# Kernel optimization log

Measured on AMD Instinct MI355X. Metric: run time of the kernel, lower is better.

Reference implementation:

```python
import jax, jax.numpy as jnp
import numpy as np
import math

H = 16
D_MODEL = 1024
D_K = D_MODEL // H


def setup_inputs() -> dict:
    key = jax.random.key(0)
    ks = jax.random.split(key, 12)
    B, S = 4, 2048
    inp = {
        "query": jax.random.normal(ks[0], (B, S, D_MODEL), jnp.float32),
        "key": jax.random.normal(ks[1], (B, S, D_MODEL), jnp.float32),
        "value": jax.random.normal(ks[2], (B, S, D_MODEL), jnp.float32),
        # causal mask, broadcastable over heads: [B, 1, S, S]
        "mask": jnp.broadcast_to(jnp.tril(jnp.ones((S, S), bool)), (B, 1, S, S)),
    }
    sc = 1.0 / math.sqrt(D_MODEL)
    inp["Wq"] = jax.random.normal(ks[3], (D_MODEL, D_MODEL), jnp.float32) * sc
    inp["bq"] = jnp.zeros((D_MODEL,), jnp.float32)
    inp["Wk"] = jax.random.normal(ks[4], (D_MODEL, D_MODEL), jnp.float32) * sc
    inp["bk"] = jnp.zeros((D_MODEL,), jnp.float32)
    inp["Wv"] = jax.random.normal(ks[5], (D_MODEL, D_MODEL), jnp.float32) * sc
    inp["bv"] = jnp.zeros((D_MODEL,), jnp.float32)
    inp["Wo"] = jax.random.normal(ks[6], (D_MODEL, D_MODEL), jnp.float32) * sc
    inp["bo"] = jnp.zeros((D_MODEL,), jnp.float32)
    return inp


def reference(query, key, value, mask, Wq, bq, Wk, bk, Wv, bv, Wo, bo):
    B, S, D = query.shape
    # torch nn.Linear: y = x @ W.T + b; then view(B,-1,h,d_k).transpose(1,2)
    def proj(x, W, b):
        return (x @ W.T + b).reshape(B, -1, H, D_K).transpose(0, 2, 1, 3)  # [B,h,S,d_k]

    q = proj(query, Wq, bq)
    k = proj(key, Wk, bk)
    v = proj(value, Wv, bv)

    scores = jnp.einsum("bhqd,bhkd->bhqk", q, k) / math.sqrt(D_K)
    scores = jnp.where(mask, scores, jnp.finfo(scores.dtype).min)
    p_attn = jax.nn.softmax(scores, axis=-1)  # dropout: eval mode (identity)
    x = jnp.einsum("bhqk,bhkd->bhqd", p_attn, v)
    x = x.transpose(0, 2, 1, 3).reshape(B, -1, H * D_K)
    return x @ Wo.T + bo
```

## Files before the change

kernel.cpp:

```cpp
#include <hip/hip_runtime.h>
#include <hip/hip_bf16.h>

typedef unsigned short u16;
typedef __attribute__((ext_vector_type(8))) short short8;
typedef __attribute__((ext_vector_type(4))) short short4v;
typedef __attribute__((ext_vector_type(4))) float f32x4;
typedef __attribute__((ext_vector_type(4))) float float4_t;

#define DIM 1024
#define NH  16
#define DKK 64
#define SEQ 2048
#define NB  4
#define SM_SCALE 0.1803368801111244f

__device__ __forceinline__ u16 f2bf(float f) {
    __bf16 h = (__bf16)f;
    return __builtin_bit_cast(u16, h);
}

__device__ __forceinline__ f32x4 mfma_bf16(short8 a, short8 b, f32x4 c) {
    return __builtin_amdgcn_mfma_f32_16x16x32_bf16(a, b, c, 0, 0, 0);
}

__device__ __forceinline__ short8 ld8_lds(const u16* p) {
    short4v lo = *(const short4v*)p;
    short4v hi = *(const short4v*)(p + 4);
    return __builtin_shufflevector(lo, hi, 0, 1, 2, 3, 4, 5, 6, 7);
}

__device__ __forceinline__ void st8_lds(u16* p, short8 v) {
    *(short4v*)p       = __builtin_shufflevector(v, v, 0, 1, 2, 3);
    *(short4v*)(p + 4) = __builtin_shufflevector(v, v, 4, 5, 6, 7);
}

__device__ __forceinline__ short8 pack8(float4_t a, float4_t b) {
    short8 v;
    v[0] = (short)f2bf(a[0]); v[1] = (short)f2bf(a[1]);
    v[2] = (short)f2bf(a[2]); v[3] = (short)f2bf(a[3]);
    v[4] = (short)f2bf(b[0]); v[5] = (short)f2bf(b[1]);
    v[6] = (short)f2bf(b[2]); v[7] = (short)f2bf(b[3]);
    return v;
}

template<int MODE>
__global__ __launch_bounds__(256)
void gemm128(const float* __restrict__ Afp, const u16* __restrict__ Abf,
             const float* __restrict__ W, const float* __restrict__ bias,
             u16* __restrict__ Cbf, float* __restrict__ Cf)
{
    __shared__ u16 As[128][40];
    __shared__ u16 Bs[128][40];
    const int tid  = threadIdx.x;
    const int lane = tid & 63;
    const int wid  = tid >> 6;
    const int wr   = wid >> 1, wc = wid & 1;
    const int m0   = blockIdx.y * 128;
    const int n0   = blockIdx.x * 128;
    const int lm   = lane & 15, lg = lane >> 4;

    f32x4 acc[4][4];
#pragma unroll
    for (int i = 0; i < 4; ++i)
#pragma unroll
        for (int j = 0; j < 4; ++j) acc[i][j] = (f32x4){0.f, 0.f, 0.f, 0.f};

    for (int k0 = 0; k0 < DIM; k0 += 32) {
#pragma unroll
        for (int it = 0; it < 2; ++it) {
            const int c   = tid + it * 256;
            const int row = c >> 2, seg = c & 3;
            short8 va;
            if (MODE == 1) {
                va = *(const short8*)(Abf + (size_t)(row + m0) * DIM + k0 + seg * 8);
            } else {
                const float* s = Afp + (size_t)(row + m0) * DIM + k0 + seg * 8;
                va = pack8(*(const float4_t*)s, *(const float4_t*)(s + 4));
            }
            st8_lds(&As[row][seg * 8], va);
            const float* sw = W + (size_t)(row + n0) * DIM + k0 + seg * 8;
            st8_lds(&Bs[row][seg * 8], pack8(*(const float4_t*)sw, *(const float4_t*)(sw + 4)));
        }
        __syncthreads();

        short8 af[4], bfr[4];
#pragma unroll
        for (int t = 0; t < 4; ++t) {
            af[t]  = ld8_lds(&As[wr * 64 + t * 16 + lm][lg * 8]);
            bfr[t] = ld8_lds(&Bs[wc * 64 + t * 16 + lm][lg * 8]);
        }
#pragma unroll
        for (int mt = 0; mt < 4; ++mt)
#pragma unroll
            for (int nt = 0; nt < 4; ++nt)
                acc[mt][nt] = mfma_bf16(af[mt], bfr[nt], acc[mt][nt]);
        __syncthreads();
    }

#pragma unroll
    for (int mt = 0; mt < 4; ++mt)
#pragma unroll
        for (int nt = 0; nt < 4; ++nt)
#pragma unroll
            for (int r = 0; r < 4; ++r) {
                const int m = m0 + wr * 64 + mt * 16 + lg * 4 + r;
                const int n = n0 + wc * 64 + nt * 16 + lm;
                if (MODE == 0) {
                    const float val = acc[mt][nt][r] + bias[n];
                    const int b = m >> 11, s = m & 2047;
                    const int h = n >> 6,  dk = n & 63;
                    Cbf[(((size_t)b * NH + h) * SEQ + s) * DKK + dk] = f2bf(val);
                } else if (MODE == 1) {
                    Cf[(size_t)m * DIM + n] = acc[mt][nt][r] + bias[n];
                } else {
                    const float val = acc[mt][nt][r] + bias[m];
                    const int h = m >> 6, dk = m & 63;
                    const int b = n >> 11, s = n & 2047;
                    Cbf[(((size_t)b * NH + h) * DKK + dk) * SEQ + s] = f2bf(val);
                }
            }
}

__global__ __launch_bounds__(256, 2)
void attn3(const u16* __restrict__ Q, const u16* __restrict__ K,
           const u16* __restrict__ Vt, u16* __restrict__ O)
{
    __shared__ __align__(16) u16 Ks[64][72];
    __shared__ __align__(16) u16 Vs[64][72];
    __shared__ __align__(16) u16 Ps[4][32][72];

    const int tid  = threadIdx.x;
    const int lane = tid & 63;
    const int w    = tid >> 6;
    const int lm   = lane & 15, lg = lane >> 4;
    const int pb   = blockIdx.x;
    const int bh   = blockIdx.y;
    const int Abase = pb * 64;
    const int Bbase = SEQ - 64 - Abase;
    const int qA = Abase + 16 * w;
    const int qB = Bbase + 16 * w;
    const u16* Qp = Q  + (size_t)bh * SEQ * DKK;
    const u16* Kp = K  + (size_t)bh * SEQ * DKK;
    const u16* Vp = Vt + (size_t)bh * DKK * SEQ;

    short8 qa[2][2];
#pragma unroll
    for (int kh = 0; kh < 2; ++kh) {
        qa[0][kh] = *(const short8*)(Qp + (size_t)(qA + lm) * DKK + kh * 32 + lg * 8);
        qa[1][kh] = *(const short8*)(Qp + (size_t)(qB + lm) * DKK + kh * 32 + lg * 8);
    }

    float m_q[2] = {-INFINITY, -INFINITY};
    float l_q[2] = {0.f, 0.f};
    f32x4 o[2][4];
#pragma unroll
    for (int qt = 0; qt < 2; ++qt)
#pragma unroll
        for (int dt = 0; dt < 4; ++dt) o[qt][dt] = (f32x4){0.f, 0.f, 0.f, 0.f};

    const f32x4 zero = (f32x4){0.f, 0.f, 0.f, 0.f};
    const int srow = tid >> 3;
    const int soct = (tid & 7) * 8;
    const int kv_end = Bbase + 64;

    short8 rk0 = *(const short8*)(Kp + (size_t)srow * DKK + soct);
    short8 rk1 = *(const short8*)(Kp + (size_t)(srow + 32) * DKK + soct);
    short8 rv0 = *(const short8*)(Vp + (size_t)srow * SEQ + soct);
    short8 rv1 = *(const short8*)(Vp + (size_t)(srow + 32) * SEQ + soct);

    for (int kv0 = 0; kv0 < kv_end; kv0 += 64) {
        __syncthreads();
        *(short8*)&Ks[srow][soct]      = rk0;
        *(short8*)&Ks[srow + 32][soct] = rk1;
        *(short8*)&Vs[srow][soct]      = rv0;
        *(short8*)&Vs[srow + 32][soct] = rv1;
        const int nkv = kv0 + 64;
        if (nkv < kv_end) {
            rk0 = *(const short8*)(Kp + (size_t)(nkv + srow) * DKK + soct);
            rk1 = *(const short8*)(Kp + (size_t)(nkv + srow + 32) * DKK + soct);
            rv0 = *(const short8*)(Vp + (size_t)srow * SEQ + nkv + soct);
            rv1 = *(const short8*)(Vp + (size_t)(srow + 32) * SEQ + nkv + soct);
        }
        __syncthreads();

        const bool actA = kv0 < qA + 16;
        const bool msk[2] = { kv0 + 63 > qA, kv0 + 63 > qB };
        const bool act[2] = { actA, true };
        const int  qb[2]  = { qA, qB };

        f32x4 s[2][4];
#pragma unroll
        for (int kvt = 0; kvt < 4; ++kvt) {
            const short8 kb0 = *(const short8*)&Ks[kvt * 16 + lm][lg * 8];
            const short8 kb1 = *(const short8*)&Ks[kvt * 16 + lm][32 + lg * 8];
            s[1][kvt] = mfma_bf16(kb1, qa[1][1], mfma_bf16(kb0, qa[1][0], zero));
            if (actA)
                s[0][kvt] = mfma_bf16(kb1, qa[0][1], mfma_bf16(kb0, qa[0][0], zero));
        }

        float mx[2] = {-INFINITY, -INFINITY};
#pragma unroll
        for (int qt = 0; qt < 2; ++qt) {
            if (!act[qt]) continue;
#pragma unroll
            for (int kvt = 0; kvt < 4; ++kvt)
#pragma unroll
                for (int r = 0; r < 4; ++r) s[qt][kvt][r] *= SM_SCALE;
            if (msk[qt]) {
                const int q = qb[qt] + lm;
#pragma unroll
                for (int kvt = 0; kvt < 4; ++kvt)
#pragma unroll
                    for (int r = 0; r < 4; ++r) {
                        const int kv = kv0 + kvt * 16 + lg * 4 + r;
                        if (kv > q) s[qt][kvt][r] = -INFINITY;
                    }
            }
            float vmax = -INFINITY;
#pragma unroll
            for (int kvt = 0; kvt < 4; ++kvt)
#pragma unroll
                for (int r = 0; r < 4; ++r) vmax = fmaxf(vmax, s[qt][kvt][r]);
            vmax = fmaxf(vmax, __shfl_xor(vmax, 16));
            vmax = fmaxf(vmax, __shfl_xor(vmax, 32));
            mx[qt] = vmax;
        }

        const bool small = (!actA || mx[0] <= m_q[0] + 8.f) && (mx[1] <= m_q[1] + 8.f);
        if (__all(small)) {
#pragma unroll
            for (int qt = 0; qt < 2; ++qt) {
                if (!act[qt]) continue;
                float ls = 0.f;
#pragma unroll
                for (int kvt = 0; kvt < 4; ++kvt) {
                    short4v pk;
#pragma unroll
                    for (int r = 0; r < 4; ++r) {
                        const float p = __builtin_exp2f(s[qt][kvt][r] - m_q[qt]);
                        ls += p;
                        pk[r] = (short)f2bf(p);
                    }
                    *(short4v*)&Ps[w][qt * 16 + lm][kvt * 16 + lg * 4] = pk;
                }
                l_q[qt] += ls;
            }
        } else {
#pragma unroll
            for (int qt = 0; qt < 2; ++qt) {
                if (!act[qt]) continue;
                const float mnew = fmaxf(m_q[qt], mx[qt]);
                const float alpha = __builtin_exp2f(m_q[qt] - mnew);
                m_q[qt] = mnew;
                float ls = 0.f;
#pragma unroll
                for (int kvt = 0; kvt < 4; ++kvt) {
                    short4v pk;
#pragma unroll
                    for (int r = 0; r < 4; ++r) {
                        const float p = __builtin_exp2f(s[qt][kvt][r] - mnew);
                        ls += p;
                        pk[r] = (short)f2bf(p);
                    }
                    *(short4v*)&Ps[w][qt * 16 + lm][kvt * 16 + lg * 4] = pk;
                }
                l_q[qt] = l_q[qt] * alpha + ls;
#pragma unroll
                for (int r = 0; r < 4; ++r) {
                    const float ar = __shfl(alpha, lg * 4 + r);
#pragma unroll
                    for (int dt = 0; dt < 4; ++dt) o[qt][dt][r] *= ar;
                }
            }
        }
        asm volatile("s_waitcnt lgkmcnt(0)" ::: "memory");

        short8 pa[2][2], vbt[4][2];
#pragma unroll
        for (int qt = 0; qt < 2; ++qt)
            if (act[qt]) {
                pa[qt][0] = *(const short8*)&Ps[w][qt * 16 + lm][lg * 8];
                pa[qt][1] = *(const short8*)&Ps[w][qt * 16 + lm][32 + lg * 8];
            }
#pragma unroll
        for (int dt = 0; dt < 4; ++dt) {
            vbt[dt][0] = *(const short8*)&Vs[dt * 16 + lm][lg * 8];
            vbt[dt][1] = *(const short8*)&Vs[dt * 16 + lm][32 + lg * 8];
        }
#pragma unroll
        for (int dt = 0; dt < 4; ++dt)
#pragma unroll
            for (int qt = 0; qt < 2; ++qt) {
                if (!act[qt]) continue;
                o[qt][dt] = mfma_bf16(pa[qt][1], vbt[dt][1],
                                      mfma_bf16(pa[qt][0], vbt[dt][0], o[qt][dt]));
            }
    }

    const int b = bh >> 4, h = bh & 15;
#pragma unroll
    for (int qt = 0; qt < 2; ++qt) {
        float lf = l_q[qt];
        lf += __shfl_xor(lf, 16);
        lf += __shfl_xor(lf, 32);
        const int qbase = qt ? qB : qA;
#pragma unroll
        for (int r = 0; r < 4; ++r) {
            const float li = 1.f / __shfl(lf, lg * 4 + r);
            const int srw = qbase + lg * 4 + r;
#pragma unroll
            for (int dt = 0; dt < 4; ++dt)
                O[(((size_t)b * SEQ + srw) * NH + h) * DKK + dt * 16 + lm] =
                    f2bf(o[qt][dt][r] * li);
        }
    }
}

extern "C" void kernel_launch(void* const* d_in, const int* in_sizes, int n_in,
                              void* d_out, int out_size, void* d_ws, size_t ws_size,
                              hipStream_t stream)
{
    const float* query = (const float*)d_in[0];
    const float* key   = (const float*)d_in[1];
    const float* value = (const float*)d_in[2];
    const float* Wq = (const float*)d_in[4];
    const float* bq = (const float*)d_in[5];
    const float* Wk = (const float*)d_in[6];
    const float* bk = (const float*)d_in[7];
    const float* Wv = (const float*)d_in[8];
    const float* bv = (const float*)d_in[9];
    const float* Wo = (const float*)d_in[10];
    const float* bo = (const float*)d_in[11];
    float* out = (float*)d_out;

    const size_t HD = (size_t)NB * NH * SEQ * DKK;
    u16* qws  = (u16*)d_ws;
    u16* kws  = qws + HD;
    u16* vtws = kws + HD;
    u16* ows  = vtws + HD;

    dim3 gg(DIM / 128, (NB * SEQ) / 128);
    dim3 gv((NB * SEQ) / 128, DIM / 128);
    gemm128<0><<<gg, 256, 0, stream>>>(query, nullptr, Wq, bq, qws, nullptr);
    gemm128<0><<<gg, 256, 0, stream>>>(key,   nullptr, Wk, bk, kws, nullptr);
    gemm128<2><<<gv, 256, 0, stream>>>(Wv, nullptr, value, bv, vtws, nullptr);
    attn3<<<dim3(SEQ / 128, NB * NH), 256, 0, stream>>>(qws, kws, vtws, ows);
    gemm128<1><<<gg, 256, 0, stream>>>(nullptr, ows, Wo, bo, nullptr, out);
}
```

Measured before the change: 264.6 us.

## Use direct global-to-LDS loads with swizzled fp32 staging in projection GEMMs

```diff
diff --git a/kernel.cpp b/kernel.cpp
--- a/kernel.cpp
+++ b/kernel.cpp
@@ -2,6 +2,7 @@
 #include <hip/hip_bf16.h>
 
 typedef unsigned short u16;
+typedef unsigned int u32;
 typedef __attribute__((ext_vector_type(8))) short short8;
 typedef __attribute__((ext_vector_type(4))) short short4v;
 typedef __attribute__((ext_vector_type(4))) float f32x4;
@@ -21,17 +22,6 @@
 
 __device__ __forceinline__ f32x4 mfma_bf16(short8 a, short8 b, f32x4 c) {
     return __builtin_amdgcn_mfma_f32_16x16x32_bf16(a, b, c, 0, 0, 0);
-}
-
-__device__ __forceinline__ short8 ld8_lds(const u16* p) {
-    short4v lo = *(const short4v*)p;
-    short4v hi = *(const short4v*)(p + 4);
-    return __builtin_shufflevector(lo, hi, 0, 1, 2, 3, 4, 5, 6, 7);
-}
-
-__device__ __forceinline__ void st8_lds(u16* p, short8 v) {
-    *(short4v*)p       = __builtin_shufflevector(v, v, 0, 1, 2, 3);
-    *(short4v*)(p + 4) = __builtin_shufflevector(v, v, 4, 5, 6, 7);
 }
 
 __device__ __forceinline__ short8 pack8(float4_t a, float4_t b) {
@@ -43,22 +33,34 @@
     return v;
 }
 
+typedef const __attribute__((address_space(1))) u32* gas1_t;
+typedef __attribute__((address_space(3))) u32* las3_t;
+__device__ __forceinline__ void g2l16(const void* g, void* l) {
+    __builtin_amdgcn_global_load_lds((gas1_t)g, (las3_t)l, 16, 0, 0);
+}
+
 template<int MODE>
 __global__ __launch_bounds__(256)
 void gemm128(const float* __restrict__ Afp, const u16* __restrict__ Abf,
              const float* __restrict__ W, const float* __restrict__ bias,
              u16* __restrict__ Cbf, float* __restrict__ Cf)
 {
-    __shared__ u16 As[128][40];
-    __shared__ u16 Bs[128][40];
+    __shared__ __align__(16) char AsRaw[MODE == 1 ? 8192 : 16384];
+    __shared__ __align__(16) float Bs[128 * 32];
+
     const int tid  = threadIdx.x;
     const int lane = tid & 63;
-    const int wid  = tid >> 6;
-    const int wr   = wid >> 1, wc = wid & 1;
+    const int w    = tid >> 6;
+    const int wr   = w >> 1, wc = w & 1;
     const int m0   = blockIdx.y * 128;
     const int n0   = blockIdx.x * 128;
     const int lm   = lane & 15, lg = lane >> 4;
 
+    const int fr = tid >> 3;
+    const int fc = (tid & 7) ^ ((tid >> 3) & 7);
+    const int hr = tid >> 2;
+    const int hc = (tid & 3) ^ ((tid >> 3) & 3);
+
     f32x4 acc[4][4];
 #pragma unroll
     for (int i = 0; i < 4; ++i)
@@ -66,35 +68,54 @@
         for (int j = 0; j < 4; ++j) acc[i][j] = (f32x4){0.f, 0.f, 0.f, 0.f};
 
     for (int k0 = 0; k0 < DIM; k0 += 32) {
-#pragma unroll
-        for (int it = 0; it < 2; ++it) {
-            const int c   = tid + it * 256;
-            const int row = c >> 2, seg = c & 3;
-            short8 va;
+        __syncthreads();
+        if (MODE == 1) {
+#pragma unroll
+            for (int c = 0; c < 2; ++c)
+                g2l16(Abf + (size_t)(m0 + c * 64 + hr) * DIM + k0 + hc * 8,
+                      AsRaw + c * 4096 + w * 1024);
+        } else {
+#pragma unroll
+            for (int c = 0; c < 4; ++c)
+                g2l16(Afp + (size_t)(m0 + c * 32 + fr) * DIM + k0 + fc * 4,
+                      AsRaw + c * 4096 + w * 1024);
+        }
+#pragma unroll
+        for (int c = 0; c < 4; ++c)
+            g2l16(W + (size_t)(n0 + c * 32 + fr) * DIM + k0 + fc * 4,
+                  (char*)Bs + c * 4096 + w * 1024);
+        __syncthreads();
+
+        short8 af[4], bfr[4];
+#pragma unroll
+        for (int t = 0; t < 4; ++t) {
+            {
+                const int R = wc * 64 + t * 16 + lm;
+                const float* rowp = Bs + R * 32;
+                const int sw = lm & 7;
+                const float4_t fa = *(const float4_t*)(rowp + ((((lg * 2)    ) ^ sw) << 2));
+                const float4_t fb = *(const float4_t*)(rowp + ((((lg * 2) | 1) ^ sw) << 2));
+                bfr[t] = pack8(fa, fb);
+            }
+            const int R = wr * 64 + t * 16 + lm;
             if (MODE == 1) {
-                va = *(const short8*)(Abf + (size_t)(row + m0) * DIM + k0 + seg * 8);
+                const u16* Ash = (const u16*)AsRaw;
+                const int ch = lg ^ ((lm >> 1) & 3);
+                af[t] = *(const short8*)(Ash + R * 32 + ch * 8);
             } else {
-                const float* s = Afp + (size_t)(row + m0) * DIM + k0 + seg * 8;
-                va = pack8(*(const float4_t*)s, *(const float4_t*)(s + 4));
-            }
-            st8_lds(&As[row][seg * 8], va);
-            const float* sw = W + (size_t)(row + n0) * DIM + k0 + seg * 8;
-            st8_lds(&Bs[row][seg * 8], pack8(*(const float4_t*)sw, *(const float4_t*)(sw + 4)));
-        }
-        __syncthreads();
-
-        short8 af[4], bfr[4];
-#pragma unroll
-        for (int t = 0; t < 4; ++t) {
-            af[t]  = ld8_lds(&As[wr * 64 + t * 16 + lm][lg * 8]);
-            bfr[t] = ld8_lds(&Bs[wc * 64 + t * 16 + lm][lg * 8]);
+                const float* Asf = (const float*)AsRaw;
+                const float* rowp = Asf + R * 32;
+                const int sw = lm & 7;
+                const float4_t fa = *(const float4_t*)(rowp + ((((lg * 2)    ) ^ sw) << 2));
+                const float4_t fb = *(const float4_t*)(rowp + ((((lg * 2) | 1) ^ sw) << 2));
+                af[t] = pack8(fa, fb);
+            }
         }
 #pragma unroll
         for (int mt = 0; mt < 4; ++mt)
 #pragma unroll
             for (int nt = 0; nt < 4; ++nt)
                 acc[mt][nt] = mfma_bf16(af[mt], bfr[nt], acc[mt][nt]);
-        __syncthreads();
     }
 
 #pragma unroll
@@ -133,8 +154,10 @@
     const int lane = tid & 63;
     const int w    = tid >> 6;
     const int lm   = lane & 15, lg = lane >> 4;
-    const int pb   = blockIdx.x;
-    const int bh   = blockIdx.y;
+    const int Lr   = blockIdx.y * gridDim.x + blockIdx.x;
+    const int work = (Lr & 7) * 128 + (Lr >> 3);
+    const int pb   = work & 15;
+    const int bh   = work >> 4;
     const int Abase = pb * 64;
     const int Bbase = SEQ - 64 - Abase;
     const int qA = Abase + 16 * w;
@@ -344,6 +367,6 @@
     gemm128<0><<<gg, 256, 0, stream>>>(query, nullptr, Wq, bq, qws, nullptr);
     gemm128<0><<<gg, 256, 0, stream>>>(key,   nullptr, Wk, bk, kws, nullptr);
     gemm128<2><<<gv, 256, 0, stream>>>(Wv, nullptr, value, bv, vtws, nullptr);
-    attn3<<<dim3(SEQ / 128, NB * NH), 256, 0, stream>>>(qws, kws, vtws, ows);
+    attn3<<<dim3(16, NB * NH), 256, 0, stream>>>(qws, kws, vtws, ows);
     gemm128<1><<<gg, 256, 0, stream>>>(nullptr, ows, Wo, bo, nullptr, out);
 }
```

Result: no change. 264.6 us (+0.0%).
